# Performance work log

Hardware: AMD Instinct MI355X
Metric: run time of the kernel (lower is better)

## Reference

```python
import jax, jax.numpy as jnp
import numpy as np

WD, WH, WW = 4, 8, 8
N_WIN = WD * WH * WW  # 256 tokens per window
NUM_HEADS = 8
DIM = 512
HIDDEN = int(DIM * 4.0)
SHIFT = (2, 4, 4)
EPS = 1e-5


def _rel_pos_index():
    coords = np.stack(np.meshgrid(np.arange(WD), np.arange(WH), np.arange(WW), indexing='ij'))
    cf = coords.reshape(3, -1)  # [3, N]
    rc = cf[:, :, None] - cf[:, None, :]  # [3, N, N]
    rc = rc.transpose(1, 2, 0).astype(np.int64)
    rc[:, :, 0] += WD - 1
    rc[:, :, 1] += WH - 1
    rc[:, :, 2] += WW - 1
    rc[:, :, 0] *= (2 * WH - 1) * (2 * WW - 1)
    rc[:, :, 1] *= (2 * WW - 1)
    return jnp.asarray(rc.sum(-1))  # [N, N]

REL_IDX = _rel_pos_index()


def setup_inputs() -> dict:
    key = jax.random.key(0)
    ks = jax.random.split(key, 10)
    B, D, H, W = 1, 16, 64, 64
    L = D * H * W
    s = 0.02
    table_size = (2 * WD - 1) * (2 * WH - 1) * (2 * WW - 1)  # 1575
    return {
        'x': jax.random.normal(ks[0], (B, L, DIM), jnp.float32),
        't_emb': jax.random.normal(ks[1], (B, DIM), jnp.float32),
        'ada_w': jax.random.normal(ks[2], (DIM, 6 * DIM), jnp.float32) * s,
        'ada_b': jnp.zeros((6 * DIM,), jnp.float32),
        'rel_table': jax.random.normal(ks[3], (table_size, NUM_HEADS), jnp.float32) * s,
        'qkv_w': jax.random.normal(ks[4], (DIM, 3 * DIM), jnp.float32) * s,
        'qkv_b': jnp.zeros((3 * DIM,), jnp.float32),
        'proj_w': jax.random.normal(ks[5], (DIM, DIM), jnp.float32) * s,
        'proj_b': jnp.zeros((DIM,), jnp.float32),
        'fc1_w': jax.random.normal(ks[6], (DIM, HIDDEN), jnp.float32) * s,
        'fc1_b': jnp.zeros((HIDDEN,), jnp.float32),
        'fc2_w': jax.random.normal(ks[7], (HIDDEN, DIM), jnp.float32) * s,
        'fc2_b': jnp.zeros((DIM,), jnp.float32),
        'D': D, 'H': H, 'W': W,
    }


def _layernorm(y):
    m = jnp.mean(y, axis=-1, keepdims=True)
    v = jnp.mean(jnp.square(y - m), axis=-1, keepdims=True)
    return (y - m) * jax.lax.rsqrt(v + EPS)


def _window_partition(x3, D, H, W):
    B, _, _, _, C = x3.shape
    x3 = x3.reshape(B, D // WD, WD, H // WH, WH, W // WW, WW, C)
    x3 = x3.transpose(0, 1, 3, 5, 2, 4, 6, 7)
    return x3.reshape(-1, N_WIN, C)


def _window_reverse(win, B, D, H, W):
    C = win.shape[-1]
    x3 = win.reshape(B, D // WD, H // WH, W // WW, WD, WH, WW, C)
    x3 = x3.transpose(0, 1, 4, 2, 5, 3, 6, 7)
    return x3.reshape(B, D, H, W, C)


def _window_attention(xn, rel_table, qkv_w, qkv_b, proj_w, proj_b):
    Bn, N, C = xn.shape
    h, d = NUM_HEADS, C // NUM_HEADS
    qkv = (xn @ qkv_w + qkv_b).reshape(Bn, N, 3, h, d).transpose(2, 0, 3, 1, 4)
    q, k, v = qkv[0], qkv[1], qkv[2]
    scale = d ** -0.5
    attn = jnp.einsum('bhnd,bhmd->bhnm', q * scale, k)  # [Bn, h, N, N]
    bias = rel_table[REL_IDX]  # gather -> [N, N, h]
    attn = jax.nn.softmax(attn + bias.transpose(2, 0, 1)[None], axis=-1)
    o = jnp.einsum('bhnm,bhmd->bhnd', attn, v)
    o = o.transpose(0, 2, 1, 3).reshape(Bn, N, C)
    return o @ proj_w + proj_b


def reference(x, t_emb, ada_w, ada_b, rel_table, qkv_w, qkv_b, proj_w, proj_b,
              fc1_w, fc1_b, fc2_w, fc2_b, D, H, W):
    B, L, C = x.shape
    mod = jax.nn.silu(t_emb) @ ada_w + ada_b  # [B, 6C]
    shift_msa, scale_msa, gate_msa, shift_mlp, scale_mlp, gate_mlp = jnp.split(mod, 6, axis=-1)

    x3 = x.reshape(B, D, H, W, C)
    x3 = jnp.roll(x3, shift=(-SHIFT[0], -SHIFT[1], -SHIFT[2]), axis=(1, 2, 3))
    xw = _window_partition(x3, D, H, W)  # [B*nW, N, C]

    xn = _layernorm(xw) * (1.0 + scale_msa[:, None, :]) + shift_msa[:, None, :]
    attn_out = _window_attention(xn, rel_table, qkv_w, qkv_b, proj_w, proj_b)
    xw = xw + gate_msa[:, None, :] * attn_out

    x3 = _window_reverse(xw, B, D, H, W)
    x3 = jnp.roll(x3, shift=SHIFT, axis=(1, 2, 3))
    x = x3.reshape(B, L, C)

    xn = _layernorm(x) * (1.0 + scale_mlp[:, None, :]) + shift_mlp[:, None, :]
    h1 = jax.nn.gelu(xn @ fc1_w + fc1_b, approximate=False)
    mlp_out = h1 @ fc2_w + fc2_b
    return x + gate_mlp[:, None, :] * mlp_out
```

## Files before the change

### kernel.cpp

```cpp
#include <hip/hip_runtime.h>
#include <hip/hip_bf16.h>
#include <math.h>


typedef __attribute__((ext_vector_type(8))) short short8;
typedef __attribute__((ext_vector_type(4))) short bs4;
typedef __attribute__((ext_vector_type(4))) float f32x4;

typedef const __attribute__((address_space(1))) unsigned int gu32;
typedef __attribute__((address_space(3))) unsigned int lu32;

__device__ __forceinline__ float bf2f(short s) {
  unsigned int u = ((unsigned int)(unsigned short)s) << 16;
  float f;
  __builtin_memcpy(&f, &u, 4);
  return f;
}
__device__ __forceinline__ short f2bf(float f) {
  unsigned int u;
  __builtin_memcpy(&u, &f, 4);
  u += 0x7FFFu + ((u >> 16) & 1u);
  return (short)(u >> 16);
}
__device__ __forceinline__ short f2bf_trunc(float f) {
  unsigned int u;
  __builtin_memcpy(&u, &f, 4);
  return (short)(u >> 16);
}

__device__ __forceinline__ int win_to_src(int p) {
  int wi = p >> 8, t = p & 255;
  int sd = (((wi >> 6) << 2) + (t >> 6) + 2) & 15;
  int sh = ((((wi >> 3) & 7) << 3) + ((t >> 3) & 7) + 4) & 63;
  int sw = (((wi & 7) << 3) + (t & 7) + 4) & 63;
  return (sd << 12) | (sh << 6) | sw;
}

__global__ __launch_bounds__(256) void mod_kernel(
    const float* __restrict__ t_emb, const float* __restrict__ ada_w,
    const float* __restrict__ ada_b, float* __restrict__ mod) {
  __shared__ float sl[512];
  int tid = threadIdx.x;
  for (int r = 0; r < 2; ++r) {
    float x = t_emb[r * 256 + tid];
    sl[r * 256 + tid] = x / (1.f + expf(-x));
  }
  __syncthreads();
  int col = blockIdx.x * 256 + tid;
  float acc = ada_b[col];
  for (int k = 0; k < 512; ++k)
    acc += sl[k] * ada_w[(size_t)k * 3072 + col];
  mod[col] = acc;
}

__global__ __launch_bounds__(256) void bias_kernel(
    const float* __restrict__ rel_table, short* __restrict__ biasT) {
  int head = blockIdx.x >> 8;
  int j = blockIdx.x & 255;
  int i = threadIdx.x;
  int di = i >> 6, hi = (i >> 3) & 7, wi = i & 7;
  int dj = j >> 6, hj = (j >> 3) & 7, wj = j & 7;
  int idx = (di - dj + 3) * 225 + (hi - hj + 7) * 15 + (wi - wj + 7);
  biasT[(size_t)blockIdx.x * 256 + i] = f2bf(rel_table[idx * 8 + head]);
}

__global__ __launch_bounds__(256) void transpose_kernel(
    const float* __restrict__ in, short* __restrict__ out, int K, int N) {
  __shared__ short t[32][33];
  int n0 = blockIdx.x * 32, k0 = blockIdx.y * 32;
  int tx = threadIdx.x & 31, ty = threadIdx.x >> 5;
#pragma unroll
  for (int r = 0; r < 4; ++r)
    t[ty + r * 8][tx] = f2bf(in[(size_t)(k0 + ty + r * 8) * N + n0 + tx]);
  __syncthreads();
#pragma unroll
  for (int r = 0; r < 4; ++r)
    out[(size_t)(n0 + ty + r * 8) * K + k0 + tx] = t[tx][ty + r * 8];
}

__global__ __launch_bounds__(256) void perm_transpose_kernel(
    const float* __restrict__ in, short* __restrict__ out) {
  __shared__ float t[64][65];
  int a = blockIdx.x;
  int kb = blockIdx.y;
  int tx = threadIdx.x & 63, ty = threadIdx.x >> 6;
#pragma unroll
  for (int r = 0; r < 16; ++r) {
    int kk = ty * 16 + r;
    t[kk][tx] = in[(size_t)(kb * 64 + kk) * 2048 + a * 64 + tx];
  }
  __syncthreads();
#pragma unroll
  for (int r = 0; r < 16; ++r) {
    int jl = ty * 16 + r;
    int lc = 4 * (jl & 15) + ((jl >> 4) & 3);
    out[(size_t)(a * 64 + jl) * 512 + kb * 64 + tx] = f2bf(t[tx][lc]);
  }
}

template <int GATHER>
__global__ __launch_bounds__(256) void ln_kernel(
    const float* __restrict__ xin, short* __restrict__ xout,
    const float* __restrict__ shv, const float* __restrict__ scv) {
  int wave = threadIdx.x >> 6, lane = threadIdx.x & 63;
  int p = blockIdx.x * 4 + wave;
  int s = GATHER ? win_to_src(p) : p;
  const f32x4* px = (const f32x4*)(xin + (size_t)s * 512 + lane * 8);
  f32x4 a = px[0], b = px[1];
  float xs[8];
#pragma unroll
  for (int j = 0; j < 4; ++j) { xs[j] = a[j]; xs[4 + j] = b[j]; }
  float sum = 0.f, sq = 0.f;
#pragma unroll
  for (int j = 0; j < 8; ++j) { sum += xs[j]; sq += xs[j] * xs[j]; }
#pragma unroll
  for (int off = 1; off < 64; off <<= 1) {
    sum += __shfl_xor(sum, off, 64);
    sq += __shfl_xor(sq, off, 64);
  }
  float mean = sum * (1.f / 512.f);
  float var = sq * (1.f / 512.f) - mean * mean;
  float rs = rsqrtf(var + 1e-5f);
  short8 o;
#pragma unroll
  for (int j = 0; j < 8; ++j) {
    int c = lane * 8 + j;
    float val = (xs[j] - mean) * rs * (1.f + scv[c]) + shv[c];
    o[j] = f2bf(val);
  }
  *(short8*)(xout + (size_t)p * 512 + lane * 8) = o;
}

template <int EPI>
__global__ __launch_bounds__(512) void gemm_kernel(
    const short* __restrict__ A, const short* __restrict__ BT,
    const float* __restrict__ bias, void* __restrict__ Cv,
    int M, int N, int K, int nbn,
    const float* __restrict__ resid, const float* __restrict__ gate) {
  __shared__ __align__(16) short Atl[256 * 64];
  __shared__ __align__(16) short Btl[128 * 64];

  int nwg = gridDim.x;
  int bid = blockIdx.x;
  int q = nwg >> 3, r = nwg & 7;
  int xcd = bid & 7, idx = bid >> 3;
  int swz = (xcd < r ? xcd * (q + 1) : r * (q + 1) + (xcd - r) * q) + idx;
  int bm = swz / nbn, bn = swz % nbn;

  int tid = threadIdx.x;
  int lane = tid & 63, wave = tid >> 6;
  int l15 = lane & 15, lg = lane >> 4;
  int wr = (wave >> 1) * 64, wc = (wave & 1) * 64;

  const size_t rowb = (size_t)K * 2;
  const char* ga[4];
  const char* gb[2];
  int loA[4], loB[2];
#pragma unroll
  for (int rr = 0; rr < 4; ++rr) {
    int o = rr * 8192 + tid * 16;
    int so = o ^ (((o >> 7) & 7) << 4);
    int row = so >> 7, cb = so & 127;
    loA[rr] = o;
    ga[rr] = (const char*)A + (size_t)(bm * 256 + row) * rowb + cb;
  }
#pragma unroll
  for (int rr = 0; rr < 2; ++rr) {
    int o = rr * 8192 + tid * 16;
    int so = o ^ (((o >> 7) & 7) << 4);
    int row = so >> 7, cb = so & 127;
    loB[rr] = o;
    gb[rr] = (const char*)BT + (size_t)(bn * 128 + row) * rowb + cb;
  }

  f32x4 acc[4][4];
#pragma unroll
  for (int m = 0; m < 4; ++m)
#pragma unroll
    for (int n = 0; n < 4; ++n) acc[m][n] = (f32x4){0.f, 0.f, 0.f, 0.f};

  const int swr = (l15 & 7) << 4;

  for (int kt = 0; kt < K; kt += 64) {
#pragma unroll
    for (int rr = 0; rr < 4; ++rr) {
      __builtin_amdgcn_global_load_lds((gu32*)ga[rr], (lu32*)((char*)Atl + loA[rr]), 16, 0, 0);
      ga[rr] += 128;
    }
#pragma unroll
    for (int rr = 0; rr < 2; ++rr) {
      __builtin_amdgcn_global_load_lds((gu32*)gb[rr], (lu32*)((char*)Btl + loB[rr]), 16, 0, 0);
      gb[rr] += 128;
    }
    __syncthreads();

    short8 af[2][4], bfr[2][4];
#pragma unroll
    for (int m = 0; m < 4; ++m) {
      int base = (wr + m * 16 + l15) * 128;
#pragma unroll
      for (int ks = 0; ks < 2; ++ks)
        af[ks][m] = *(const short8*)((const char*)Atl + base + ((ks * 64 + lg * 16) ^ swr));
    }
#pragma unroll
    for (int n = 0; n < 4; ++n) {
      int base = (wc + n * 16 + l15) * 128;
#pragma unroll
      for (int ks = 0; ks < 2; ++ks)
        bfr[ks][n] = *(const short8*)((const char*)Btl + base + ((ks * 64 + lg * 16) ^ swr));
    }
#pragma unroll
    for (int ks = 0; ks < 2; ++ks)
#pragma unroll
      for (int m = 0; m < 4; ++m)
#pragma unroll
        for (int n = 0; n < 4; ++n)
          acc[m][n] = __builtin_amdgcn_mfma_f32_16x16x32_bf16(af[ks][m], bfr[ks][n], acc[m][n], 0, 0, 0);
    __syncthreads();
  }

  if (EPI == 1) {
    int colb = bn * 128 + wc + 4 * l15;
    f32x4 bv4 = *(const f32x4*)(bias + colb);
#pragma unroll
    for (int m = 0; m < 4; ++m)
#pragma unroll
      for (int i = 0; i < 4; ++i) {
        int row = bm * 256 + wr + m * 16 + lg * 4 + i;
        bs4 pk;
#pragma unroll
        for (int n = 0; n < 4; ++n) {
          float v = acc[m][n][i] + bv4[n];
          float tt = v * (0.7978845608f + 0.0356774081f * v * v);
          float sg = 1.f / (1.f + __expf(-2.f * tt));
          pk[n] = f2bf_trunc(v * sg);
        }
        *(bs4*)((short*)Cv + (size_t)row * N + colb) = pk;
      }
  } else {
#pragma unroll
    for (int m = 0; m < 4; ++m)
#pragma unroll
      for (int n = 0; n < 4; ++n) {
        int col = bn * 128 + wc + n * 16 + l15;
        float bv = bias[col];
#pragma unroll
        for (int i = 0; i < 4; ++i) {
          int row = bm * 256 + wr + m * 16 + lg * 4 + i;
          float v = acc[m][n][i] + bv;
          if (EPI == 0) {
            if (col < 512) v *= 0.125f;
            ((short*)Cv)[(size_t)row * N + col] = f2bf_trunc(v);
          } else if (EPI == 2) {
            int s = win_to_src(row);
            float xv = resid[(size_t)s * 512 + col];
            ((float*)Cv)[(size_t)s * 512 + col] = xv + gate[col] * v;
          } else {
            float xv = resid[(size_t)row * 512 + col];
            ((float*)Cv)[(size_t)row * 512 + col] = xv + gate[col] * v;
          }
        }
      }
  }
}

__global__ __launch_bounds__(256) void attn_kernel(
    const short* __restrict__ qkv, const short* __restrict__ biasT,
    short* __restrict__ aout) {
  __shared__ __align__(16) short vt[64][264];
  __shared__ __align__(16) short pl[4][64][40];
  int win = blockIdx.x, head = blockIdx.y;
  int tid = threadIdx.x, lane = tid & 63, wave = tid >> 6;
  int l15 = lane & 15, lg = lane >> 4;
  const short* qp = qkv + (size_t)win * 256 * 1536 + head * 64;
  const short* kp = qp + 512;
  const short* vp = qp + 1024;

#pragma unroll
  for (int r = 0; r < 8; ++r) {
    short8 vv = *(const short8*)(vp + (size_t)tid * 1536 + r * 8);
#pragma unroll
    for (int j = 0; j < 8; ++j) vt[r * 8 + j][tid] = vv[j];
  }

  short8 qf[4][2];
#pragma unroll
  for (int m = 0; m < 4; ++m)
#pragma unroll
    for (int kk = 0; kk < 2; ++kk)
      qf[m][kk] = *(const short8*)(qp + (size_t)(wave * 64 + m * 16 + l15) * 1536 + kk * 32 + lg * 8);

  __syncthreads();

  float lsum[4][4];
  f32x4 ao[4][4];
#pragma unroll
  for (int m = 0; m < 4; ++m)
#pragma unroll
    for (int i = 0; i < 4; ++i) lsum[m][i] = 0.f;
#pragma unroll
  for (int m = 0; m < 4; ++m)
#pragma unroll
    for (int n = 0; n < 4; ++n) ao[m][n] = (f32x4){0.f, 0.f, 0.f, 0.f};

  for (int kc = 0; kc < 4; ++kc) {
    f32x4 sv[4][4];
#pragma unroll
    for (int m = 0; m < 4; ++m)
#pragma unroll
      for (int n = 0; n < 4; ++n) sv[m][n] = (f32x4){0.f, 0.f, 0.f, 0.f};
#pragma unroll
    for (int n = 0; n < 4; ++n)
#pragma unroll
      for (int kk = 0; kk < 2; ++kk) {
        short8 kf = *(const short8*)(kp + (size_t)(kc * 64 + n * 16 + l15) * 1536 + kk * 32 + lg * 8);
#pragma unroll
        for (int m = 0; m < 4; ++m)
          sv[m][n] = __builtin_amdgcn_mfma_f32_16x16x32_bf16(qf[m][kk], kf, sv[m][n], 0, 0, 0);
      }
#pragma unroll
    for (int n = 0; n < 4; ++n) {
      const short* bq = biasT + (size_t)(head * 256 + kc * 64 + n * 16 + l15) * 256 + wave * 64 + lg * 4;
#pragma unroll
      for (int m = 0; m < 4; ++m) {
        bs4 bt = *(const bs4*)(bq + m * 16);
#pragma unroll
        for (int i = 0; i < 4; ++i) {
          float pe = __expf(sv[m][n][i] + bf2f(bt[i]));
          sv[m][n][i] = pe;
          lsum[m][i] += pe;
        }
      }
    }
#pragma unroll
    for (int s = 0; s < 2; ++s) {
#pragma unroll
      for (int m = 0; m < 4; ++m)
#pragma unroll
        for (int nn = 0; nn < 2; ++nn) {
          int n = 2 * s + nn;
#pragma unroll
          for (int i = 0; i < 4; ++i)
            pl[wave][m * 16 + lg * 4 + i][nn * 16 + l15] = f2bf_trunc(sv[m][n][i]);
        }
      short8 pf[4];
#pragma unroll
      for (int m = 0; m < 4; ++m)
        pf[m] = *(const short8*)&pl[wave][m * 16 + l15][lg * 8];
#pragma unroll
      for (int n2 = 0; n2 < 4; ++n2) {
        short8 vf = *(const short8*)&vt[n2 * 16 + l15][kc * 64 + s * 32 + lg * 8];
#pragma unroll
        for (int m = 0; m < 4; ++m)
          ao[m][n2] = __builtin_amdgcn_mfma_f32_16x16x32_bf16(pf[m], vf, ao[m][n2], 0, 0, 0);
      }
    }
  }

#pragma unroll
  for (int m = 0; m < 4; ++m)
#pragma unroll
    for (int i = 0; i < 4; ++i) {
#pragma unroll
      for (int off = 1; off < 16; off <<= 1)
        lsum[m][i] += __shfl_xor(lsum[m][i], off, 64);
    }

#pragma unroll
  for (int m = 0; m < 4; ++m)
#pragma unroll
    for (int i = 0; i < 4; ++i) {
      float inv = 1.f / lsum[m][i];
      int row = win * 256 + wave * 64 + m * 16 + lg * 4 + i;
#pragma unroll
      for (int n = 0; n < 4; ++n)
        aout[(size_t)row * 512 + head * 64 + n * 16 + l15] = f2bf(ao[m][n][i] * inv);
    }
}

extern "C" void kernel_launch(void* const* d_in, const int* in_sizes, int n_in,
                              void* d_out, int out_size, void* d_ws, size_t ws_size,
                              hipStream_t stream) {
  (void)in_sizes; (void)n_in; (void)out_size; (void)ws_size;
  const float* x         = (const float*)d_in[0];
  const float* t_emb     = (const float*)d_in[1];
  const float* ada_w     = (const float*)d_in[2];
  const float* ada_b     = (const float*)d_in[3];
  const float* rel_table = (const float*)d_in[4];
  const float* qkv_w     = (const float*)d_in[5];
  const float* qkv_b     = (const float*)d_in[6];
  const float* proj_w    = (const float*)d_in[7];
  const float* proj_b    = (const float*)d_in[8];
  const float* fc1_w     = (const float*)d_in[9];
  const float* fc1_b     = (const float*)d_in[10];
  const float* fc2_w     = (const float*)d_in[11];
  const float* fc2_b     = (const float*)d_in[12];
  float* out = (float*)d_out;
  char* ws = (char*)d_ws;

  float* mod    = (float*)(ws);
  short* biasT  = (short*)(ws + 16384);
  short* qkvwT  = (short*)(ws + 16384 + 2097152);
  short* projwT = qkvwT + 1536 * 512;
  short* fc1wT  = projwT + 512 * 512;
  short* fc2wT  = fc1wT + 2048 * 512;
  short* xn     = (short*)(ws + 8404992);
  short* qkvb   = xn + (size_t)65536 * 512;
  short* attno  = qkvb + (size_t)65536 * 1536;
  short* h1     = qkvb;
  float* x2     = out;

  mod_kernel<<<12, 256, 0, stream>>>(t_emb, ada_w, ada_b, mod);
  bias_kernel<<<2048, 256, 0, stream>>>(rel_table, biasT);
  transpose_kernel<<<dim3(48, 16), 256, 0, stream>>>(qkv_w, qkvwT, 512, 1536);
  transpose_kernel<<<dim3(16, 16), 256, 0, stream>>>(proj_w, projwT, 512, 512);
  perm_transpose_kernel<<<dim3(32, 8), 256, 0, stream>>>(fc1_w, fc1wT);
  transpose_kernel<<<dim3(16, 64), 256, 0, stream>>>(fc2_w, fc2wT, 2048, 512);

  ln_kernel<1><<<16384, 256, 0, stream>>>(x, xn, mod + 0, mod + 512);
  gemm_kernel<0><<<256 * 12, 512, 0, stream>>>(xn, qkvwT, qkv_b, qkvb,
                                               65536, 1536, 512, 12, nullptr, nullptr);
  attn_kernel<<<dim3(256, 8), 256, 0, stream>>>(qkvb, biasT, attno);
  gemm_kernel<2><<<256 * 4, 512, 0, stream>>>(attno, projwT, proj_b, x2,
                                              65536, 512, 512, 4, x, mod + 1024);
  ln_kernel<0><<<16384, 256, 0, stream>>>(x2, xn, mod + 1536, mod + 2048);
  gemm_kernel<1><<<256 * 16, 512, 0, stream>>>(xn, fc1wT, fc1_b, h1,
                                               65536, 2048, 512, 16, nullptr, nullptr);
  gemm_kernel<3><<<256 * 4, 512, 0, stream>>>(h1, fc2wT, fc2_b, out,
                                              65536, 512, 2048, 4, x2, mod + 2560);
}
```

Baseline: 873.4 us.

## Permute all weight columns for vectorized GEMM epilogues; widen attention to 8 waves

Every weight transpose now goes through the permuted transpose, so each lane owns four adjacent output columns in all GEMMs. The QKV and residual epilogues can then load bias, gate and residual and store results as 4-wide vectors instead of scalars. The attention kernel moves from 4 to 8 waves per block, with each wave covering 32 query rows, to raise occupancy and lower register pressure. In exchange, each block reloads the K fragments and bias rows across more waves, and the column permutation must line up exactly with the epilogue indexing.

```diff
diff --git a/kernel.cpp b/kernel.cpp
--- a/kernel.cpp
+++ b/kernel.cpp
@@ -64,22 +64,8 @@
   biasT[(size_t)blockIdx.x * 256 + i] = f2bf(rel_table[idx * 8 + head]);
 }
 
-__global__ __launch_bounds__(256) void transpose_kernel(
-    const float* __restrict__ in, short* __restrict__ out, int K, int N) {
-  __shared__ short t[32][33];
-  int n0 = blockIdx.x * 32, k0 = blockIdx.y * 32;
-  int tx = threadIdx.x & 31, ty = threadIdx.x >> 5;
-#pragma unroll
-  for (int r = 0; r < 4; ++r)
-    t[ty + r * 8][tx] = f2bf(in[(size_t)(k0 + ty + r * 8) * N + n0 + tx]);
-  __syncthreads();
-#pragma unroll
-  for (int r = 0; r < 4; ++r)
-    out[(size_t)(n0 + ty + r * 8) * K + k0 + tx] = t[tx][ty + r * 8];
-}
-
 __global__ __launch_bounds__(256) void perm_transpose_kernel(
-    const float* __restrict__ in, short* __restrict__ out) {
+    const float* __restrict__ in, short* __restrict__ out, int Nin, int K) {
   __shared__ float t[64][65];
   int a = blockIdx.x;
   int kb = blockIdx.y;
@@ -87,14 +73,14 @@
 #pragma unroll
   for (int r = 0; r < 16; ++r) {
     int kk = ty * 16 + r;
-    t[kk][tx] = in[(size_t)(kb * 64 + kk) * 2048 + a * 64 + tx];
+    t[kk][tx] = in[(size_t)(kb * 64 + kk) * Nin + a * 64 + tx];
   }
   __syncthreads();
 #pragma unroll
   for (int r = 0; r < 16; ++r) {
     int jl = ty * 16 + r;
     int lc = 4 * (jl & 15) + ((jl >> 4) & 3);
-    out[(size_t)(a * 64 + jl) * 512 + kb * 64 + tx] = f2bf(t[tx][lc]);
+    out[(size_t)(a * 64 + jl) * K + kb * 64 + tx] = f2bf(t[tx][lc]);
   }
 }
 
@@ -219,9 +205,21 @@
     __syncthreads();
   }
 
-  if (EPI == 1) {
-    int colb = bn * 128 + wc + 4 * l15;
-    f32x4 bv4 = *(const f32x4*)(bias + colb);
+  int colb = bn * 128 + wc + 4 * l15;
+  f32x4 bv4 = *(const f32x4*)(bias + colb);
+  if (EPI == 0) {
+    float sc = (colb < 512) ? 0.125f : 1.f;
+#pragma unroll
+    for (int m = 0; m < 4; ++m)
+#pragma unroll
+      for (int i = 0; i < 4; ++i) {
+        int row = bm * 256 + wr + m * 16 + lg * 4 + i;
+        bs4 pk;
+#pragma unroll
+        for (int n = 0; n < 4; ++n) pk[n] = f2bf_trunc((acc[m][n][i] + bv4[n]) * sc);
+        *(bs4*)((short*)Cv + (size_t)row * N + colb) = pk;
+      }
+  } else if (EPI == 1) {
 #pragma unroll
     for (int m = 0; m < 4; ++m)
 #pragma unroll
@@ -238,37 +236,27 @@
         *(bs4*)((short*)Cv + (size_t)row * N + colb) = pk;
       }
   } else {
+    f32x4 gv = *(const f32x4*)(gate + colb);
 #pragma unroll
     for (int m = 0; m < 4; ++m)
 #pragma unroll
-      for (int n = 0; n < 4; ++n) {
-        int col = bn * 128 + wc + n * 16 + l15;
-        float bv = bias[col];
-#pragma unroll
-        for (int i = 0; i < 4; ++i) {
-          int row = bm * 256 + wr + m * 16 + lg * 4 + i;
-          float v = acc[m][n][i] + bv;
-          if (EPI == 0) {
-            if (col < 512) v *= 0.125f;
-            ((short*)Cv)[(size_t)row * N + col] = f2bf_trunc(v);
-          } else if (EPI == 2) {
-            int s = win_to_src(row);
-            float xv = resid[(size_t)s * 512 + col];
-            ((float*)Cv)[(size_t)s * 512 + col] = xv + gate[col] * v;
-          } else {
-            float xv = resid[(size_t)row * 512 + col];
-            ((float*)Cv)[(size_t)row * 512 + col] = xv + gate[col] * v;
-          }
-        }
-      }
-  }
-}
-
-__global__ __launch_bounds__(256) void attn_kernel(
+      for (int i = 0; i < 4; ++i) {
+        int row = bm * 256 + wr + m * 16 + lg * 4 + i;
+        int s = (EPI == 2) ? win_to_src(row) : row;
+        f32x4 rv = *(const f32x4*)(resid + (size_t)s * 512 + colb);
+        f32x4 o;
+#pragma unroll
+        for (int n = 0; n < 4; ++n) o[n] = rv[n] + gv[n] * (acc[m][n][i] + bv4[n]);
+        *(f32x4*)((float*)Cv + (size_t)s * 512 + colb) = o;
+      }
+  }
+}
+
+__global__ __launch_bounds__(512) void attn_kernel(
     const short* __restrict__ qkv, const short* __restrict__ biasT,
     short* __restrict__ aout) {
   __shared__ __align__(16) short vt[64][264];
-  __shared__ __align__(16) short pl[4][64][40];
+  __shared__ __align__(16) short pl[8][32][40];
   int win = blockIdx.x, head = blockIdx.y;
   int tid = threadIdx.x, lane = tid & 63, wave = tid >> 6;
   int l15 = lane & 15, lg = lane >> 4;
@@ -276,37 +264,38 @@
   const short* kp = qp + 512;
   const short* vp = qp + 1024;
 
-#pragma unroll
-  for (int r = 0; r < 8; ++r) {
-    short8 vv = *(const short8*)(vp + (size_t)tid * 1536 + r * 8);
-#pragma unroll
-    for (int j = 0; j < 8; ++j) vt[r * 8 + j][tid] = vv[j];
-  }
-
-  short8 qf[4][2];
-#pragma unroll
-  for (int m = 0; m < 4; ++m)
+  int key = tid >> 1, dh = (tid & 1) * 32;
+#pragma unroll
+  for (int r = 0; r < 4; ++r) {
+    short8 vv = *(const short8*)(vp + (size_t)key * 1536 + dh + r * 8);
+#pragma unroll
+    for (int j = 0; j < 8; ++j) vt[dh + r * 8 + j][key] = vv[j];
+  }
+
+  short8 qf[2][2];
+#pragma unroll
+  for (int m = 0; m < 2; ++m)
 #pragma unroll
     for (int kk = 0; kk < 2; ++kk)
-      qf[m][kk] = *(const short8*)(qp + (size_t)(wave * 64 + m * 16 + l15) * 1536 + kk * 32 + lg * 8);
+      qf[m][kk] = *(const short8*)(qp + (size_t)(wave * 32 + m * 16 + l15) * 1536 + kk * 32 + lg * 8);
 
   __syncthreads();
 
-  float lsum[4][4];
-  f32x4 ao[4][4];
-#pragma unroll
-  for (int m = 0; m < 4; ++m)
+  float lsum[2][4];
+  f32x4 ao[2][4];
+#pragma unroll
+  for (int m = 0; m < 2; ++m)
 #pragma unroll
     for (int i = 0; i < 4; ++i) lsum[m][i] = 0.f;
 #pragma unroll
-  for (int m = 0; m < 4; ++m)
+  for (int m = 0; m < 2; ++m)
 #pragma unroll
     for (int n = 0; n < 4; ++n) ao[m][n] = (f32x4){0.f, 0.f, 0.f, 0.f};
 
   for (int kc = 0; kc < 4; ++kc) {
-    f32x4 sv[4][4];
-#pragma unroll
-    for (int m = 0; m < 4; ++m)
+    f32x4 sv[2][4];
+#pragma unroll
+    for (int m = 0; m < 2; ++m)
 #pragma unroll
       for (int n = 0; n < 4; ++n) sv[m][n] = (f32x4){0.f, 0.f, 0.f, 0.f};
 #pragma unroll
@@ -315,14 +304,14 @@
       for (int kk = 0; kk < 2; ++kk) {
         short8 kf = *(const short8*)(kp + (size_t)(kc * 64 + n * 16 + l15) * 1536 + kk * 32 + lg * 8);
 #pragma unroll
-        for (int m = 0; m < 4; ++m)
+        for (int m = 0; m < 2; ++m)
           sv[m][n] = __builtin_amdgcn_mfma_f32_16x16x32_bf16(qf[m][kk], kf, sv[m][n], 0, 0, 0);
       }
 #pragma unroll
     for (int n = 0; n < 4; ++n) {
-      const short* bq = biasT + (size_t)(head * 256 + kc * 64 + n * 16 + l15) * 256 + wave * 64 + lg * 4;
-#pragma unroll
-      for (int m = 0; m < 4; ++m) {
+      const short* bq = biasT + (size_t)(head * 256 + kc * 64 + n * 16 + l15) * 256 + wave * 32 + lg * 4;
+#pragma unroll
+      for (int m = 0; m < 2; ++m) {
         bs4 bt = *(const bs4*)(bq + m * 16);
 #pragma unroll
         for (int i = 0; i < 4; ++i) {
@@ -335,7 +324,7 @@
 #pragma unroll
     for (int s = 0; s < 2; ++s) {
 #pragma unroll
-      for (int m = 0; m < 4; ++m)
+      for (int m = 0; m < 2; ++m)
 #pragma unroll
         for (int nn = 0; nn < 2; ++nn) {
           int n = 2 * s + nn;
@@ -343,22 +332,22 @@
           for (int i = 0; i < 4; ++i)
             pl[wave][m * 16 + lg * 4 + i][nn * 16 + l15] = f2bf_trunc(sv[m][n][i]);
         }
-      short8 pf[4];
-#pragma unroll
-      for (int m = 0; m < 4; ++m)
+      short8 pf[2];
+#pragma unroll
+      for (int m = 0; m < 2; ++m)
         pf[m] = *(const short8*)&pl[wave][m * 16 + l15][lg * 8];
 #pragma unroll
       for (int n2 = 0; n2 < 4; ++n2) {
         short8 vf = *(const short8*)&vt[n2 * 16 + l15][kc * 64 + s * 32 + lg * 8];
 #pragma unroll
-        for (int m = 0; m < 4; ++m)
+        for (int m = 0; m < 2; ++m)
           ao[m][n2] = __builtin_amdgcn_mfma_f32_16x16x32_bf16(pf[m], vf, ao[m][n2], 0, 0, 0);
       }
     }
   }
 
 #pragma unroll
-  for (int m = 0; m < 4; ++m)
+  for (int m = 0; m < 2; ++m)
 #pragma unroll
     for (int i = 0; i < 4; ++i) {
 #pragma unroll
@@ -367,11 +356,11 @@
     }
 
 #pragma unroll
-  for (int m = 0; m < 4; ++m)
+  for (int m = 0; m < 2; ++m)
 #pragma unroll
     for (int i = 0; i < 4; ++i) {
       float inv = 1.f / lsum[m][i];
-      int row = win * 256 + wave * 64 + m * 16 + lg * 4 + i;
+      int row = win * 256 + wave * 32 + m * 16 + lg * 4 + i;
 #pragma unroll
       for (int n = 0; n < 4; ++n)
         aout[(size_t)row * 512 + head * 64 + n * 16 + l15] = f2bf(ao[m][n][i] * inv);
@@ -412,15 +401,15 @@
 
   mod_kernel<<<12, 256, 0, stream>>>(t_emb, ada_w, ada_b, mod);
   bias_kernel<<<2048, 256, 0, stream>>>(rel_table, biasT);
-  transpose_kernel<<<dim3(48, 16), 256, 0, stream>>>(qkv_w, qkvwT, 512, 1536);
-  transpose_kernel<<<dim3(16, 16), 256, 0, stream>>>(proj_w, projwT, 512, 512);
-  perm_transpose_kernel<<<dim3(32, 8), 256, 0, stream>>>(fc1_w, fc1wT);
-  transpose_kernel<<<dim3(16, 64), 256, 0, stream>>>(fc2_w, fc2wT, 2048, 512);
+  perm_transpose_kernel<<<dim3(24, 8), 256, 0, stream>>>(qkv_w, qkvwT, 1536, 512);
+  perm_transpose_kernel<<<dim3(8, 8), 256, 0, stream>>>(proj_w, projwT, 512, 512);
+  perm_transpose_kernel<<<dim3(32, 8), 256, 0, stream>>>(fc1_w, fc1wT, 2048, 512);
+  perm_transpose_kernel<<<dim3(8, 32), 256, 0, stream>>>(fc2_w, fc2wT, 512, 2048);
 
   ln_kernel<1><<<16384, 256, 0, stream>>>(x, xn, mod + 0, mod + 512);
   gemm_kernel<0><<<256 * 12, 512, 0, stream>>>(xn, qkvwT, qkv_b, qkvb,
                                                65536, 1536, 512, 12, nullptr, nullptr);
-  attn_kernel<<<dim3(256, 8), 256, 0, stream>>>(qkvb, biasT, attno);
+  attn_kernel<<<dim3(256, 8), 512, 0, stream>>>(qkvb, biasT, attno);
   gemm_kernel<2><<<256 * 4, 512, 0, stream>>>(attno, projwT, proj_b, x2,
                                               65536, 512, 512, 4, x, mod + 1024);
   ln_kernel<0><<<16384, 256, 0, stream>>>(x2, xn, mod + 1536, mod + 2048);
```

Result: faster. 846.1 us, median of 4 (-3.1%).
